# Kernel tuning notes

Measured on AMD Instinct MI355X. Metric: run time of the kernel, lower is better.

## Reference

```python
import jax, jax.numpy as jnp
import numpy as np

N = 500_000   # num nodes
F = 128       # num_features
H = 128       # hidden
B = 32_768    # batch size
K = 4         # hops
RWS = 16      # random walks per batch node
E = RWS * B   # sampled edges per hop
ALPHA = 0.1
OUT = 8


def setup_inputs() -> dict:
    key = jax.random.key(0)
    ks = jax.random.split(key, 12)
    x = jax.random.normal(ks[0], (N, F), dtype=jnp.float32)
    degree = jax.random.uniform(ks[1], (N,), dtype=jnp.float32, minval=1.0, maxval=64.0)
    batch = jax.random.randint(ks[2], (B,), 0, N, dtype=jnp.int32)
    heads_idx = jax.random.randint(ks[3], (K, E), 0, B, dtype=jnp.int32)
    ends = jax.random.randint(ks[4], (K, E), 0, N, dtype=jnp.int32)
    # MLP params (Kaiming-ish scaling)
    W0 = jax.random.normal(ks[5], (F, H), dtype=jnp.float32) / np.float32(np.sqrt(F))
    b0 = jnp.zeros((H,), dtype=jnp.float32)
    W1 = jax.random.normal(ks[6], (H, H), dtype=jnp.float32) / np.float32(np.sqrt(H))
    b1 = jnp.zeros((H,), dtype=jnp.float32)
    W2 = jax.random.normal(ks[7], (H, OUT), dtype=jnp.float32) / np.float32(np.sqrt(H))
    b2 = jnp.zeros((OUT,), dtype=jnp.float32)
    # APPNP attention weights: alpha*(1-alpha)^k, last = (1-alpha)^K
    att = np.float32(ALPHA) * np.float32(1.0 - ALPHA) ** np.arange(K + 1, dtype=np.float32)
    att[-1] = np.float32(1.0 - ALPHA) ** np.float32(K)
    att = jnp.asarray(att)
    return {"x": x, "W0": W0, "b0": b0, "W1": W1, "b1": b1, "W2": W2, "b2": b2,
            "att": att, "degree": degree, "batch": batch,
            "heads_idx": heads_idx, "ends": ends}


def reference(x, W0, b0, W1, b1, W2, b2, att, degree, batch, heads_idx, ends):
    # eval mode: dropout is a no-op
    dis = degree ** -0.5  # deg_inv_sqrt

    def mlp(feats):  # lins[1](relu(lins[0](feats)))
        h = jax.nn.relu(feats @ W0 + b0)
        return h @ W1 + b1

    nb = batch.shape[0]
    ne = jnp.float32(ends.shape[1])
    dsum = degree[batch].sum()

    aggx = att[0] * mlp(x[batch])                       # [B, H]
    for k in range(K):  # small fixed hop count
        heads = heads_idx[k]                            # local rows in [0, B)
        e = ends[k]                                     # global node ids
        val = dis[batch[heads]] * dis[e] * (dsum / ne)  # [E]
        tmp = mlp(x[e]) * val[:, None]                  # gather + MLP + weight
        aggx = aggx + att[k + 1] * jax.ops.segment_sum(tmp, heads, num_segments=nb)
    out = jax.nn.relu(aggx) @ W2 + b2                   # [B, 8]
    return jax.nn.log_softmax(out, axis=1)
```

## Files before the change

### kernel.cpp

```cpp
#include <hip/hip_runtime.h>

#define NN 500000
#define FF 128
#define HH 128
#define BB 32768
#define KHOPS 4
#define EPER 524288
#define KE (KHOPS * EPER)
#define NOUT 8
#define SBLK 256
#define EPB (KE / SBLK)

typedef unsigned short u16;
typedef unsigned char u8;
typedef __attribute__((ext_vector_type(8))) short short8v;
typedef __attribute__((ext_vector_type(4))) float f32x4;

__device__ __forceinline__ float bflo(unsigned int u) {
    union { unsigned int x; float f; } t; t.x = u << 16; return t.f;
}
__device__ __forceinline__ float bfhi(unsigned int u) {
    union { unsigned int x; float f; } t; t.x = u & 0xFFFF0000u; return t.f;
}
__device__ __forceinline__ u16 f2bf(float f) {
    union { float f; unsigned int u; } t; t.f = f;
    unsigned int u = t.u;
    unsigned int r = (u + 0x7FFFu + ((u >> 16) & 1u)) >> 16;
    return (u16)r;
}

__global__ void k_degsum1(const float* __restrict__ deg, const int* __restrict__ batch,
                          float* __restrict__ partial) {
    __shared__ float red[256];
    int i = blockIdx.x * 256 + threadIdx.x;
    red[threadIdx.x] = deg[batch[i]];
    __syncthreads();
    for (int off = 128; off > 0; off >>= 1) {
        if (threadIdx.x < off) red[threadIdx.x] += red[threadIdx.x + off];
        __syncthreads();
    }
    if (threadIdx.x == 0) partial[blockIdx.x] = red[0];
}
__global__ void k_degsum2(const float* __restrict__ partial, float* __restrict__ dsum) {
    __shared__ float red[128];
    red[threadIdx.x] = partial[threadIdx.x];
    __syncthreads();
    for (int off = 64; off > 0; off >>= 1) {
        if (threadIdx.x < off) red[threadIdx.x] += red[threadIdx.x + off];
        __syncthreads();
    }
    if (threadIdx.x == 0) *dsum = red[0];
}

__global__ void k_prep(const float* __restrict__ deg, const int* __restrict__ batch,
                       const float* __restrict__ dsum,
                       float* __restrict__ dis, float* __restrict__ disb) {
    int i = blockIdx.x * 256 + threadIdx.x;
    if (i < NN) dis[i] = rsqrtf(deg[i]);
    if (i < BB) disb[i] = rsqrtf(deg[batch[i]]) * (dsum[0] * (1.0f / (float)EPER));
}

__launch_bounds__(256, 2)
__global__ void k_hist2(const int* __restrict__ heads, u8* __restrict__ M) {
    __shared__ unsigned int hp[8192];
    int tid = threadIdx.x, blk = blockIdx.x;
    #pragma unroll
    for (int j = 0; j < 32; j++) hp[tid + j * 256] = 0;
    __syncthreads();
    int ebase = blk * EPB;
    #pragma unroll 4
    for (int it = 0; it < EPB / 256; it++) {
        int b = heads[ebase + it * 256 + tid];
        atomicAdd(&hp[b >> 2], 1u << ((b & 3) * 8));
    }
    __syncthreads();
    unsigned int* M32 = (unsigned int*)(M + (size_t)blk * BB);
    #pragma unroll
    for (int j = 0; j < 32; j++) {
        int w = tid + j * 256;
        M32[w] = hp[w];
    }
}

__global__ void k_colscan(u8* __restrict__ M, int* __restrict__ colsum) {
    int key = blockIdx.x * 256 + threadIdx.x;
    unsigned int run = 0;
    #pragma unroll 8
    for (int b = 0; b < SBLK; b++) {
        size_t idx = (size_t)b * BB + key;
        u8 v = M[idx];
        M[idx] = (u8)run;
        run += v;
    }
    colsum[key] = (int)run;
}

__global__ void k_scan(const int* __restrict__ colsum, int* __restrict__ base) {
    __shared__ int sc[1024];
    int tid = threadIdx.x;
    int loc[32];
    int run = 0;
    #pragma unroll
    for (int j = 0; j < 32; j++) {
        loc[j] = run;
        run += colsum[tid * 32 + j];
    }
    sc[tid] = run;
    __syncthreads();
    for (int off = 1; off < 1024; off <<= 1) {
        int v = (tid >= off) ? sc[tid - off] : 0;
        __syncthreads();
        sc[tid] += v;
        __syncthreads();
    }
    int excl = sc[tid] - run;
    #pragma unroll
    for (int j = 0; j < 32; j++) base[tid * 32 + j] = excl + loc[j];
    if (tid == 1023) base[BB] = sc[1023];
}

__launch_bounds__(256, 2)
__global__ void k_scatter2(const int* __restrict__ heads, const int* __restrict__ ends,
                           const u8* __restrict__ M, const int* __restrict__ base,
                           unsigned int* __restrict__ pe) {
    __shared__ unsigned int hp[8192];
    int tid = threadIdx.x, blk = blockIdx.x;
    #pragma unroll
    for (int j = 0; j < 32; j++) hp[tid + j * 256] = 0;
    __syncthreads();
    int ebase = blk * EPB;
    for (int it = 0; it < EPB / 256; it++) {
        int i = ebase + it * 256 + tid;
        int b = heads[i];
        unsigned int e = (unsigned int)ends[i];
        unsigned int kk = (unsigned int)(i >> 19);
        unsigned int old = atomicAdd(&hp[b >> 2], 1u << ((b & 3) * 8));
        unsigned int rank = (old >> ((b & 3) * 8)) & 0xFFu;
        int pos = base[b] + (int)M[(size_t)blk * BB + b] + (int)rank;
        pe[pos] = (kk << 19) | e;
    }
}

__global__ void k_packW0(const float* __restrict__ W0, u16* __restrict__ w0p) {
    int f = blockIdx.x * 256 + threadIdx.x;
    int k = f >> 7, c = f & 127;
    int kt = k >> 5, i = k & 7, lh = (k >> 3) & 3;
    int lane = lh * 16 + (c & 15), n = c >> 4;
    w0p[(((kt * 8 + n) * 64 + lane) << 3) + i] = f2bf(W0[f]);
}

__launch_bounds__(256, 2)
__global__ void k_gemm1(const float* __restrict__ x, const u16* __restrict__ w0p,
                        const float* __restrict__ b0, u16* __restrict__ h) {
    __shared__ u16 ws[16384];
    int tid = threadIdx.x;
    int wid = tid >> 6;
    int lane = tid & 63;
    long rowbase = (long)blockIdx.x * 128;

    #pragma unroll
    for (int r = 0; r < 8; r++) {
        int f = tid + r * 256;
        *(float4*)&ws[f * 8] = *(const float4*)&w0p[f * 8];
    }

    short8v a[2][4];
    int qc = (lane >> 4) * 8;
    #pragma unroll
    for (int rs = 0; rs < 2; rs++) {
        long grow = rowbase + wid * 32 + rs * 16 + (lane & 15);
        if (grow >= NN) grow = NN - 1;
        const float* xr = &x[grow * 128 + qc];
        #pragma unroll
        for (int kt = 0; kt < 4; kt++) {
            float4 v0 = *(const float4*)&xr[kt * 32];
            float4 v1 = *(const float4*)&xr[kt * 32 + 4];
            short8v f;
            f[0] = (short)f2bf(v0.x); f[1] = (short)f2bf(v0.y);
            f[2] = (short)f2bf(v0.z); f[3] = (short)f2bf(v0.w);
            f[4] = (short)f2bf(v1.x); f[5] = (short)f2bf(v1.y);
            f[6] = (short)f2bf(v1.z); f[7] = (short)f2bf(v1.w);
            a[rs][kt] = f;
        }
    }
    __syncthreads();

    f32x4 acc[2][8] = {};
    #pragma unroll
    for (int n = 0; n < 8; n++) {
        short8v bfr[4];
        #pragma unroll
        for (int kt = 0; kt < 4; kt++)
            bfr[kt] = *(const short8v*)&ws[(((kt * 8 + n) * 64 + lane) << 3)];
        #pragma unroll
        for (int rs = 0; rs < 2; rs++) {
            #pragma unroll
            for (int kt = 0; kt < 4; kt++)
                acc[rs][n] = __builtin_amdgcn_mfma_f32_16x16x32_bf16(
                                 a[rs][kt], bfr[kt], acc[rs][n], 0, 0, 0);
        }
    }

    float b0v[8];
    #pragma unroll
    for (int n = 0; n < 8; n++) b0v[n] = b0[n * 16 + (lane & 15)];

    __syncthreads();
    u16* xw = &ws[wid * 32 * 128];
    #pragma unroll
    for (int rs = 0; rs < 2; rs++) {
        #pragma unroll
        for (int r = 0; r < 4; r++) {
            int row = rs * 16 + (lane >> 4) * 4 + r;
            int sw = (row & 7) << 4;
            #pragma unroll
            for (int n = 0; n < 8; n++) {
                float v = acc[rs][n][r] + b0v[n];
                v = v > 0.f ? v : 0.f;
                int byte = row * 256 + ((n * 32 + (lane & 15) * 2) ^ sw);
                *(u16*)((char*)xw + byte) = f2bf(v);
            }
        }
    }
    __syncthreads();
    #pragma unroll
    for (int pass = 0; pass < 8; pass++) {
        int off = pass * 1024 + lane * 16;
        int row = off >> 8;
        int colb = off & 255;
        int ocolb = colb ^ ((row & 7) << 4);
        long grow = rowbase + wid * 32 + row;
        uint4 v = *(const uint4*)((const char*)xw + off);
        if (grow < NN)
            *(uint4*)((char*)&h[grow * 128] + ocolb) = v;
    }
}

__launch_bounds__(256)
__global__ void k_gather(const u16* __restrict__ h, const int* __restrict__ batch,
                         const int* __restrict__ base, const unsigned int* __restrict__ pe,
                         const float* __restrict__ dis, const float* __restrict__ disb,
                         const float* __restrict__ att,
                         float* __restrict__ P, float* __restrict__ s) {
    int b = blockIdx.x * 4 + (threadIdx.x >> 6);
    int l = threadIdx.x & 63;
    int q = l >> 4;
    int c8 = (l & 15) * 8;
    float att0 = att[0];
    float a1 = att[1], a2 = att[2], a3 = att[3], a4 = att[4];
    float dbv = disb[b];
    float acc[8] = {0.f, 0.f, 0.f, 0.f, 0.f, 0.f, 0.f, 0.f};

    if (q == 0) {
        int nb = batch[b];
        uint4 v = *(const uint4*)&h[(size_t)nb * 128 + c8];
        acc[0] = att0 * bflo(v.x); acc[1] = att0 * bfhi(v.x);
        acc[2] = att0 * bflo(v.y); acc[3] = att0 * bfhi(v.y);
        acc[4] = att0 * bflo(v.z); acc[5] = att0 * bfhi(v.z);
        acc[6] = att0 * bflo(v.w); acc[7] = att0 * bfhi(v.w);
    }

    int beg = base[b], fin = base[b + 1];
    float wsum = 0.f;
    for (int j = beg; j < fin; j += 32) {
        unsigned int p[8];
        #pragma unroll
        for (int u = 0; u < 8; u++) {
            int je = j + u * 4 + q;
            int jc = je < fin ? je : beg;
            p[u] = pe[jc];
            if (je >= fin) p[u] |= 0x80000000u;
        }
        float wv[8];
        uint4 v[8];
        #pragma unroll
        for (int u = 0; u < 8; u++) {
            int e = (int)(p[u] & 0x7FFFFu);
            int kk = (int)((p[u] >> 19) & 3u);
            float av = (kk < 2) ? (kk == 0 ? a1 : a2) : (kk == 2 ? a3 : a4);
            float w = av * dbv * dis[e];
            wv[u] = (p[u] & 0x80000000u) ? 0.f : w;
            v[u] = *(const uint4*)&h[(size_t)e * 128 + c8];
        }
        #pragma unroll
        for (int u = 0; u < 8; u++) {
            float w = wv[u];
            acc[0] += w * bflo(v[u].x); acc[1] += w * bfhi(v[u].x);
            acc[2] += w * bflo(v[u].y); acc[3] += w * bfhi(v[u].y);
            acc[4] += w * bflo(v[u].z); acc[5] += w * bfhi(v[u].z);
            acc[6] += w * bflo(v[u].w); acc[7] += w * bfhi(v[u].w);
            wsum += w;
        }
    }
    #pragma unroll
    for (int k = 0; k < 8; k++) {
        acc[k] += __shfl_xor(acc[k], 16);
        acc[k] += __shfl_xor(acc[k], 32);
    }
    wsum += __shfl_xor(wsum, 16);
    wsum += __shfl_xor(wsum, 32);

    if (q == 0) {
        float4 o0 = { acc[0], acc[1], acc[2], acc[3] };
        float4 o1 = { acc[4], acc[5], acc[6], acc[7] };
        *(float4*)&P[(size_t)b * 128 + c8]     = o0;
        *(float4*)&P[(size_t)b * 128 + c8 + 4] = o1;
        if (l == 0) s[b] = att0 + wsum;
    }
}

__launch_bounds__(256, 2)
__global__ void k_out(const float* __restrict__ P, const float* __restrict__ s,
                      const float* __restrict__ W1, const float* __restrict__ b1,
                      const float* __restrict__ W2, const float* __restrict__ b2,
                      float* __restrict__ out) {
    __shared__ float W1s[128 * 128];
    __shared__ float Ps[32 * 128];
    int tid = threadIdx.x;
    int rowbase = blockIdx.x * 32;
    #pragma unroll
    for (int rep = 0; rep < 16; rep++) {
        int f = tid + rep * 256;
        *(float4*)&W1s[f * 4] = *(const float4*)&W1[f * 4];
    }
    #pragma unroll
    for (int rep = 0; rep < 4; rep++) {
        int f = tid + rep * 256;
        *(float4*)&Ps[f * 4] = *(const float4*)&P[(size_t)rowbase * 128 + f * 4];
    }
    __syncthreads();

    int c0 = (tid & 31) * 4;
    int r0 = (tid >> 5) * 4;
    float b1r[4] = { b1[c0], b1[c0 + 1], b1[c0 + 2], b1[c0 + 3] };
    float sv[4];
    #pragma unroll
    for (int j = 0; j < 4; j++) sv[j] = s[rowbase + r0 + j];

    float acc[4][4] = {};
    #pragma unroll 2
    for (int i = 0; i < 128; i += 4) {
        float4 xq[4], wq4[4];
        #pragma unroll
        for (int j = 0; j < 4; j++) xq[j]  = *(const float4*)&Ps[(r0 + j) * 128 + i];
        #pragma unroll
        for (int q = 0; q < 4; q++) wq4[q] = *(const float4*)&W1s[(i + q) * 128 + c0];
        #pragma unroll
        for (int j = 0; j < 4; j++) {
            float xv[4] = { xq[j].x, xq[j].y, xq[j].z, xq[j].w };
            #pragma unroll
            for (int q = 0; q < 4; q++) {
                acc[j][0] += xv[q] * wq4[q].x;
                acc[j][1] += xv[q] * wq4[q].y;
                acc[j][2] += xv[q] * wq4[q].z;
                acc[j][3] += xv[q] * wq4[q].w;
            }
        }
    }
    __syncthreads();
    #pragma unroll
    for (int j = 0; j < 4; j++) {
        #pragma unroll
        for (int c = 0; c < 4; c++) {
            float v = acc[j][c] + sv[j] * b1r[c];
            Ps[(r0 + j) * 128 + c0 + c] = v > 0.f ? v : 0.f;
        }
    }
    __syncthreads();

    int row = tid >> 3;
    int o = tid & 7;
    int rot = (row * 4) & 127;
    float v = b2[o];
    #pragma unroll 4
    for (int ii = 0; ii < 128; ii++) {
        int i = (ii + rot) & 127;
        v += Ps[row * 128 + i] * W2[i * 8 + o];
    }
    float m = v;
    for (int d = 1; d < 8; d <<= 1) m = fmaxf(m, __shfl_xor(m, d, 8));
    float ex = expf(v - m);
    float sum = ex;
    for (int d = 1; d < 8; d <<= 1) sum += __shfl_xor(sum, d, 8);
    out[(size_t)(rowbase + row) * 8 + o] = (v - m) - logf(sum);
}

extern "C" void kernel_launch(void* const* d_in, const int* in_sizes, int n_in,
                              void* d_out, int out_size, void* d_ws, size_t ws_size,
                              hipStream_t stream) {
    const float* x     = (const float*)d_in[0];
    const float* W0    = (const float*)d_in[1];
    const float* b0    = (const float*)d_in[2];
    const float* W1    = (const float*)d_in[3];
    const float* b1    = (const float*)d_in[4];
    const float* W2    = (const float*)d_in[5];
    const float* b2    = (const float*)d_in[6];
    const float* att   = (const float*)d_in[7];
    const float* deg   = (const float*)d_in[8];
    const int*   batch = (const int*)d_in[9];
    const int*   heads = (const int*)d_in[10];
    const int*   ends  = (const int*)d_in[11];
    float* out = (float*)d_out;

    char* w = (char*)d_ws;
    size_t off = 0;
    u16* h = (u16*)(w + off);          off += (size_t)NN * 128 * 2;
    float* P = (float*)(w + off);      off += (size_t)BB * 128 * 4;
    float* s = (float*)(w + off);      off += (size_t)BB * 4;
    int* base = (int*)(w + off);       off += 131328;
    unsigned int* pe = (unsigned int*)(w + off); off += (size_t)KE * 4;
    u8* M = (u8*)(w + off);            off += (size_t)SBLK * BB;
    int* colsum = (int*)(w + off);     off += (size_t)BB * 4;
    float* dis = (float*)(w + off);    off += (size_t)NN * 4;
    float* disb = (float*)(w + off);   off += (size_t)BB * 4;
    float* partial = (float*)(w + off); off += 1024;
    float* dsum = (float*)(w + off);   off += 256;
    u16* w0p = (u16*)(w + off);        off += 16384 * 2;

    k_degsum1<<<128, 256, 0, stream>>>(deg, batch, partial);
    k_degsum2<<<1, 128, 0, stream>>>(partial, dsum);
    k_prep<<<(NN + 255) / 256, 256, 0, stream>>>(deg, batch, dsum, dis, disb);
    k_hist2<<<SBLK, 256, 0, stream>>>(heads, M);
    k_colscan<<<BB / 256, 256, 0, stream>>>(M, colsum);
    k_scan<<<1, 1024, 0, stream>>>(colsum, base);
    k_scatter2<<<SBLK, 256, 0, stream>>>(heads, ends, M, base, pe);
    k_packW0<<<64, 256, 0, stream>>>(W0, w0p);
    k_gemm1<<<(NN + 127) / 128, 256, 0, stream>>>(x, w0p, b0, h);
    k_gather<<<BB / 4, 256, 0, stream>>>(h, batch, base, pe, dis, disb, att, P, s);
    k_out<<<BB / 32, 256, 0, stream>>>(P, s, W1, b1, W2, b2, out);
}
```

Measured before the change: 307.6 us.

## Restructure gather so each wavefront lane owns two columns and shuffles edge indices

The gather kernel now has each lane of the 64-wide wavefront own two bf16 columns of the 128-wide row. Edge indices and weights are loaded once per 32-edge chunk, one per lane, and broadcast with shuffles, so each edge row is fetched as one coalesced 256-byte read by the whole wave. Previously four sub-groups each handled different edges with 16-byte loads and were combined by a cross-lane reduction at the end. This removes that final reduction and the duplicated index loads, but adds 64 shuffles per chunk, 32 outstanding 4-byte loads per lane, and a separate 32-wide shuffle per half-wave.

```diff
diff --git a/kernel.cpp b/kernel.cpp
--- a/kernel.cpp
+++ b/kernel.cpp
@@ -244,69 +244,46 @@
                          float* __restrict__ P, float* __restrict__ s) {
     int b = blockIdx.x * 4 + (threadIdx.x >> 6);
     int l = threadIdx.x & 63;
-    int q = l >> 4;
-    int c8 = (l & 15) * 8;
+    int l32 = l & 31;
     float att0 = att[0];
     float a1 = att[1], a2 = att[2], a3 = att[3], a4 = att[4];
     float dbv = disb[b];
-    float acc[8] = {0.f, 0.f, 0.f, 0.f, 0.f, 0.f, 0.f, 0.f};
-
-    if (q == 0) {
-        int nb = batch[b];
-        uint4 v = *(const uint4*)&h[(size_t)nb * 128 + c8];
-        acc[0] = att0 * bflo(v.x); acc[1] = att0 * bfhi(v.x);
-        acc[2] = att0 * bflo(v.y); acc[3] = att0 * bfhi(v.y);
-        acc[4] = att0 * bflo(v.z); acc[5] = att0 * bfhi(v.z);
-        acc[6] = att0 * bflo(v.w); acc[7] = att0 * bfhi(v.w);
-    }
+
+    int nb = batch[b];
+    unsigned int v0 = *(const unsigned int*)((const char*)h + ((size_t)nb << 8) + l * 4);
+    float accx = att0 * bflo(v0);
+    float accy = att0 * bfhi(v0);
+    float wsum = 0.f;
 
     int beg = base[b], fin = base[b + 1];
-    float wsum = 0.f;
     for (int j = beg; j < fin; j += 32) {
-        unsigned int p[8];
-        #pragma unroll
-        for (int u = 0; u < 8; u++) {
-            int je = j + u * 4 + q;
-            int jc = je < fin ? je : beg;
-            p[u] = pe[jc];
-            if (je >= fin) p[u] |= 0x80000000u;
-        }
-        float wv[8];
-        uint4 v[8];
-        #pragma unroll
-        for (int u = 0; u < 8; u++) {
-            int e = (int)(p[u] & 0x7FFFFu);
-            int kk = (int)((p[u] >> 19) & 3u);
-            float av = (kk < 2) ? (kk == 0 ? a1 : a2) : (kk == 2 ? a3 : a4);
-            float w = av * dbv * dis[e];
-            wv[u] = (p[u] & 0x80000000u) ? 0.f : w;
-            v[u] = *(const uint4*)&h[(size_t)e * 128 + c8];
-        }
-        #pragma unroll
-        for (int u = 0; u < 8; u++) {
-            float w = wv[u];
-            acc[0] += w * bflo(v[u].x); acc[1] += w * bfhi(v[u].x);
-            acc[2] += w * bflo(v[u].y); acc[3] += w * bfhi(v[u].y);
-            acc[4] += w * bflo(v[u].z); acc[5] += w * bfhi(v[u].z);
-            acc[6] += w * bflo(v[u].w); acc[7] += w * bfhi(v[u].w);
-            wsum += w;
-        }
-    }
-    #pragma unroll
-    for (int k = 0; k < 8; k++) {
-        acc[k] += __shfl_xor(acc[k], 16);
-        acc[k] += __shfl_xor(acc[k], 32);
-    }
-    wsum += __shfl_xor(wsum, 16);
-    wsum += __shfl_xor(wsum, 32);
-
-    if (q == 0) {
-        float4 o0 = { acc[0], acc[1], acc[2], acc[3] };
-        float4 o1 = { acc[4], acc[5], acc[6], acc[7] };
-        *(float4*)&P[(size_t)b * 128 + c8]     = o0;
-        *(float4*)&P[(size_t)b * 128 + c8 + 4] = o1;
-        if (l == 0) s[b] = att0 + wsum;
-    }
+        int jc = j + l32;
+        int jl = jc < fin ? jc : beg;
+        unsigned int p = pe[jl];
+        int e = (int)(p & 0x7FFFFu);
+        int kk = (int)(p >> 19);
+        float av = (kk < 2) ? (kk == 0 ? a1 : a2) : (kk == 2 ? a3 : a4);
+        float wv = av * dbv * dis[e];
+        if (jc >= fin) wv = 0.f;
+
+        unsigned int v[32];
+        #pragma unroll
+        for (int u = 0; u < 32; u++) {
+            int eu = __shfl(e, u, 32);
+            v[u] = *(const unsigned int*)((const char*)h + ((size_t)(unsigned)eu << 8) + l * 4);
+        }
+        #pragma unroll
+        for (int u = 0; u < 32; u++) {
+            float wu = __shfl(wv, u, 32);
+            accx += wu * bflo(v[u]);
+            accy += wu * bfhi(v[u]);
+            wsum += wu;
+        }
+    }
+
+    float2 o = { accx, accy };
+    *(float2*)&P[(size_t)b * 128 + l * 2] = o;
+    if (l == 0) s[b] = att0 + wsum;
 }
 
 __launch_bounds__(256, 2)
```

Result: no change. 312.4 us (+1.6%).

## Merge preprocessing kernels into three multi-role launches and pack column scan

Applied to the files above, without the earlier changes.

Replaces the degree-sum, dis/disb prep, histogram, column scan, global scan and W0 packing kernels with three launches. Each launch assigns different roles to different block ranges, so independent work runs side by side and fewer small launches are issued before the scatter. The column scan now works on four byte counters packed in one 32-bit word per thread, so each thread scans four keys at once. This relies on the per-key running counts staying below 256 so no carry crosses byte lanes, and colsum is now truncated to 8 bits.

```diff
diff --git a/kernel.cpp b/kernel.cpp
--- a/kernel.cpp
+++ b/kernel.cpp
@@ -29,94 +29,119 @@
     return (u16)r;
 }
 
-__global__ void k_degsum1(const float* __restrict__ deg, const int* __restrict__ batch,
-                          float* __restrict__ partial) {
-    __shared__ float red[256];
-    int i = blockIdx.x * 256 + threadIdx.x;
-    red[threadIdx.x] = deg[batch[i]];
-    __syncthreads();
-    for (int off = 128; off > 0; off >>= 1) {
-        if (threadIdx.x < off) red[threadIdx.x] += red[threadIdx.x + off];
+__launch_bounds__(256, 2)
+__global__ void k_preA(const int* __restrict__ heads, u8* __restrict__ M,
+                       const float* __restrict__ deg, const int* __restrict__ batch,
+                       float* __restrict__ partial, float* __restrict__ dis) {
+    __shared__ unsigned int hp[8192];
+    int tid = threadIdx.x;
+    int bid = blockIdx.x;
+    if (bid < SBLK) {
+        #pragma unroll
+        for (int j = 0; j < 32; j++) hp[tid + j * 256] = 0;
         __syncthreads();
-    }
-    if (threadIdx.x == 0) partial[blockIdx.x] = red[0];
-}
-__global__ void k_degsum2(const float* __restrict__ partial, float* __restrict__ dsum) {
-    __shared__ float red[128];
-    red[threadIdx.x] = partial[threadIdx.x];
-    __syncthreads();
-    for (int off = 64; off > 0; off >>= 1) {
-        if (threadIdx.x < off) red[threadIdx.x] += red[threadIdx.x + off];
+        int ebase = bid * EPB;
+        #pragma unroll 4
+        for (int it = 0; it < EPB / 256; it++) {
+            int b = heads[ebase + it * 256 + tid];
+            atomicAdd(&hp[b >> 2], 1u << ((b & 3) * 8));
+        }
         __syncthreads();
-    }
-    if (threadIdx.x == 0) *dsum = red[0];
-}
-
-__global__ void k_prep(const float* __restrict__ deg, const int* __restrict__ batch,
-                       const float* __restrict__ dsum,
-                       float* __restrict__ dis, float* __restrict__ disb) {
-    int i = blockIdx.x * 256 + threadIdx.x;
-    if (i < NN) dis[i] = rsqrtf(deg[i]);
-    if (i < BB) disb[i] = rsqrtf(deg[batch[i]]) * (dsum[0] * (1.0f / (float)EPER));
-}
-
-__launch_bounds__(256, 2)
-__global__ void k_hist2(const int* __restrict__ heads, u8* __restrict__ M) {
-    __shared__ unsigned int hp[8192];
-    int tid = threadIdx.x, blk = blockIdx.x;
-    #pragma unroll
-    for (int j = 0; j < 32; j++) hp[tid + j * 256] = 0;
-    __syncthreads();
-    int ebase = blk * EPB;
-    #pragma unroll 4
-    for (int it = 0; it < EPB / 256; it++) {
-        int b = heads[ebase + it * 256 + tid];
-        atomicAdd(&hp[b >> 2], 1u << ((b & 3) * 8));
-    }
-    __syncthreads();
-    unsigned int* M32 = (unsigned int*)(M + (size_t)blk * BB);
-    #pragma unroll
-    for (int j = 0; j < 32; j++) {
-        int w = tid + j * 256;
-        M32[w] = hp[w];
-    }
-}
-
-__global__ void k_colscan(u8* __restrict__ M, int* __restrict__ colsum) {
-    int key = blockIdx.x * 256 + threadIdx.x;
-    unsigned int run = 0;
-    #pragma unroll 8
-    for (int b = 0; b < SBLK; b++) {
-        size_t idx = (size_t)b * BB + key;
-        u8 v = M[idx];
-        M[idx] = (u8)run;
-        run += v;
-    }
-    colsum[key] = (int)run;
-}
-
-__global__ void k_scan(const int* __restrict__ colsum, int* __restrict__ base) {
-    __shared__ int sc[1024];
+        unsigned int* M32 = (unsigned int*)(M + (size_t)bid * BB);
+        #pragma unroll
+        for (int j = 0; j < 32; j++) {
+            int w = tid + j * 256;
+            M32[w] = hp[w];
+        }
+    } else if (bid < SBLK + 128) {
+        float* red = (float*)hp;
+        int i = (bid - SBLK) * 256 + tid;
+        red[tid] = deg[batch[i]];
+        __syncthreads();
+        for (int off = 128; off > 0; off >>= 1) {
+            if (tid < off) red[tid] += red[tid + off];
+            __syncthreads();
+        }
+        if (tid == 0) partial[bid - SBLK] = red[0];
+    } else {
+        int i0 = (bid - SBLK - 128) * 1024 + tid * 4;
+        if (i0 < NN) {
+            float4 d = *(const float4*)&deg[i0];
+            float4 o;
+            o.x = rsqrtf(d.x); o.y = rsqrtf(d.y);
+            o.z = rsqrtf(d.z); o.w = rsqrtf(d.w);
+            *(float4*)&dis[i0] = o;
+        }
+    }
+}
+
+__global__ void k_preB(const float* __restrict__ partial, float* __restrict__ dsum,
+                       u8* __restrict__ M, int* __restrict__ colsum) {
     int tid = threadIdx.x;
-    int loc[32];
-    int run = 0;
-    #pragma unroll
-    for (int j = 0; j < 32; j++) {
-        loc[j] = run;
-        run += colsum[tid * 32 + j];
-    }
-    sc[tid] = run;
-    __syncthreads();
-    for (int off = 1; off < 1024; off <<= 1) {
-        int v = (tid >= off) ? sc[tid - off] : 0;
+    if (blockIdx.x == 0) {
+        __shared__ float red[128];
+        if (tid < 128) red[tid] = partial[tid];
         __syncthreads();
-        sc[tid] += v;
+        for (int off = 64; off > 0; off >>= 1) {
+            if (tid < off) red[tid] += red[tid + off];
+            __syncthreads();
+        }
+        if (tid == 0) dsum[0] = red[0];
+    } else {
+        int g = (blockIdx.x - 1) * 256 + tid;
+        unsigned int* M32 = (unsigned int*)M;
+        unsigned int run = 0;
+        #pragma unroll 8
+        for (int b = 0; b < SBLK; b++) {
+            size_t idx = (size_t)b * (BB / 4) + g;
+            unsigned int v = M32[idx];
+            M32[idx] = run;
+            run += v;
+        }
+        colsum[g * 4 + 0] = (int)(run & 0xFFu);
+        colsum[g * 4 + 1] = (int)((run >> 8) & 0xFFu);
+        colsum[g * 4 + 2] = (int)((run >> 16) & 0xFFu);
+        colsum[g * 4 + 3] = (int)((run >> 24) & 0xFFu);
+    }
+}
+
+__global__ void k_preC(const int* __restrict__ colsum, int* __restrict__ base,
+                       const float* __restrict__ deg, const int* __restrict__ batch,
+                       const float* __restrict__ dsum, float* __restrict__ disb,
+                       const float* __restrict__ W0, u16* __restrict__ w0p) {
+    int tid = threadIdx.x;
+    if (blockIdx.x == 0) {
+        __shared__ int sc[1024];
+        int loc[32];
+        int run = 0;
+        #pragma unroll
+        for (int j = 0; j < 32; j++) {
+            loc[j] = run;
+            run += colsum[tid * 32 + j];
+        }
+        sc[tid] = run;
         __syncthreads();
-    }
-    int excl = sc[tid] - run;
-    #pragma unroll
-    for (int j = 0; j < 32; j++) base[tid * 32 + j] = excl + loc[j];
-    if (tid == 1023) base[BB] = sc[1023];
+        for (int off = 1; off < 1024; off <<= 1) {
+            int v = (tid >= off) ? sc[tid - off] : 0;
+            __syncthreads();
+            sc[tid] += v;
+            __syncthreads();
+        }
+        int excl = sc[tid] - run;
+        #pragma unroll
+        for (int j = 0; j < 32; j++) base[tid * 32 + j] = excl + loc[j];
+        if (tid == 1023) base[BB] = sc[1023];
+    } else if (blockIdx.x <= 32) {
+        int b = (blockIdx.x - 1) * 1024 + tid;
+        float sc2 = dsum[0] * (1.0f / (float)EPER);
+        disb[b] = rsqrtf(deg[batch[b]]) * sc2;
+    } else {
+        int f = (blockIdx.x - 33) * 1024 + tid;
+        int k = f >> 7, c = f & 127;
+        int kt = k >> 5, i = k & 7, lh = (k >> 3) & 3;
+        int lane = lh * 16 + (c & 15), n = c >> 4;
+        w0p[(((kt * 8 + n) * 64 + lane) << 3) + i] = f2bf(W0[f]);
+    }
 }
 
 __launch_bounds__(256, 2)
@@ -139,14 +164,6 @@
         int pos = base[b] + (int)M[(size_t)blk * BB + b] + (int)rank;
         pe[pos] = (kk << 19) | e;
     }
-}
-
-__global__ void k_packW0(const float* __restrict__ W0, u16* __restrict__ w0p) {
-    int f = blockIdx.x * 256 + threadIdx.x;
-    int k = f >> 7, c = f & 127;
-    int kt = k >> 5, i = k & 7, lh = (k >> 3) & 3;
-    int lane = lh * 16 + (c & 15), n = c >> 4;
-    w0p[(((kt * 8 + n) * 64 + lane) << 3) + i] = f2bf(W0[f]);
 }
 
 __launch_bounds__(256, 2)
@@ -417,14 +434,12 @@
     float* dsum = (float*)(w + off);   off += 256;
     u16* w0p = (u16*)(w + off);        off += 16384 * 2;
 
-    k_degsum1<<<128, 256, 0, stream>>>(deg, batch, partial);
-    k_degsum2<<<1, 128, 0, stream>>>(partial, dsum);
-    k_prep<<<(NN + 255) / 256, 256, 0, stream>>>(deg, batch, dsum, dis, disb);
-    k_hist2<<<SBLK, 256, 0, stream>>>(heads, M);
-    k_colscan<<<BB / 256, 256, 0, stream>>>(M, colsum);
-    k_scan<<<1, 1024, 0, stream>>>(colsum, base);
+    int disBlocks = (NN + 1023) / 1024;
+    k_preA<<<SBLK + 128 + disBlocks, 256, 0, stream>>>(heads, M, deg, batch,
+                                                       partial, dis);
+    k_preB<<<33, 256, 0, stream>>>(partial, dsum, M, colsum);
+    k_preC<<<49, 1024, 0, stream>>>(colsum, base, deg, batch, dsum, disb, W0, w0p);
     k_scatter2<<<SBLK, 256, 0, stream>>>(heads, ends, M, base, pe);
-    k_packW0<<<64, 256, 0, stream>>>(W0, w0p);
     k_gemm1<<<(NN + 127) / 128, 256, 0, stream>>>(x, w0p, b0, h);
     k_gather<<<BB / 4, 256, 0, stream>>>(h, batch, base, pe, dis, disb, att, P, s);
     k_out<<<BB / 32, 256, 0, stream>>>(P, s, W1, b1, W2, b2, out);
```

After: 298.7 us, median of 2. 1.03x faster.
